# Kernel optimization log

Hardware: AMD Instinct MI355X
Metric: run time of the kernel (lower is better)

The kernel has to match this reference:

```python
import jax, jax.numpy as jnp
import numpy as np

T, N, H = 20, 1000000, 20  # timesteps, num_params (batch), lstm hidden dim


def setup_inputs() -> dict:
    key = jax.random.key(0)
    ks = jax.random.split(key, 7)
    s = 1.0 / np.sqrt(H)  # pytorch LSTM/Linear init scale (uniform bound); use gaussian of similar scale
    return {
        "grads": jax.random.normal(ks[0], (T, N), dtype=jnp.float32),
        "w_ih": jax.random.normal(ks[1], (4 * H, 1), dtype=jnp.float32) * s,
        "w_hh": jax.random.normal(ks[2], (4 * H, H), dtype=jnp.float32) * s,
        "b_ih": jax.random.normal(ks[3], (4 * H,), dtype=jnp.float32) * s,
        "b_hh": jax.random.normal(ks[4], (4 * H,), dtype=jnp.float32) * s,
        "w_fc": jax.random.normal(ks[5], (1, H), dtype=jnp.float32) * s,
        "b_fc": jax.random.normal(ks[6], (1,), dtype=jnp.float32) * s,
    }


def reference(grads, w_ih, w_hh, b_ih, b_hh, w_fc, b_fc):
    # grads: [T, N]; coordinate-wise LSTM: batch = N, input_size = 1, hidden = H.
    # PyTorch LSTM gate order: i, f, g, o.
    n = grads.shape[1]
    bias = b_ih + b_hh  # [4H]
    w_ih_v = w_ih[:, 0]  # [4H], input size is 1

    def step(carry, x_t):
        h, c = carry  # [N, H] each
        # gates: [N, 4H]
        gates = x_t[:, None] * w_ih_v[None, :] + h @ w_hh.T + bias
        i, f, g, o = jnp.split(gates, 4, axis=1)
        c_new = jax.nn.sigmoid(f) * c + jax.nn.sigmoid(i) * jnp.tanh(g)
        h_new = jax.nn.sigmoid(o) * jnp.tanh(c_new)
        out_t = h_new @ w_fc.T + b_fc  # [N, 1]
        return (h_new, c_new), out_t[:, 0]

    h0 = jnp.zeros((n, w_hh.shape[1]), dtype=grads.dtype)
    c0 = jnp.zeros((n, w_hh.shape[1]), dtype=grads.dtype)
    _, outs = jax.lax.scan(step, (h0, c0), grads)
    return outs  # [T, N], matches torch.cat(outputs) of [1, N] slices
```

## Files before the change

kernel.cpp:

```cpp
#include <hip/hip_runtime.h>

#define TT 20
#define HH 20

typedef float f32x4 __attribute__((ext_vector_type(4)));
typedef short bf16x8 __attribute__((ext_vector_type(8)));
typedef unsigned uint4v __attribute__((ext_vector_type(4)));

__device__ __forceinline__ short f2bf(float f) {
    unsigned u = __float_as_uint(f);
    unsigned r = (u + 0x7fffu + ((u >> 16) & 1u)) >> 16;
    return (short)r;
}

__device__ __forceinline__ unsigned pk_bf16(float a, float b) {
    unsigned r;
    asm("v_cvt_pk_bf16_f32 %0, %1, %2" : "=v"(r) : "v"(a), "v"(b));
    return r;
}

__device__ __forceinline__ void build_B(const float (&hn)[5][4], const float (&xv)[4],
                                        float xm, float om, bf16x8 (&Bhi)[4])
{
    #pragma unroll
    for (int b = 0; b < 4; ++b) {
        const float s7 = fmaf(xm, xv[b], om);
        uint4v uh;
        uh[0] = pk_bf16(hn[0][b], hn[1][b]);
        uh[1] = pk_bf16(hn[2][b], hn[3][b]);
        uh[2] = pk_bf16(hn[4][b], 0.0f);
        uh[3] = pk_bf16(0.0f, s7);
        Bhi[b] = __builtin_bit_cast(bf16x8, uh);
    }
}

__device__ __forceinline__ void nonlin(const f32x4 a, float& cst, float& hout,
                                       const float TLOG2E)
{
    const float ei = __builtin_amdgcn_exp2f(a[0]);
    const float ef = __builtin_amdgcn_exp2f(a[1]);
    const float eg = __builtin_amdgcn_exp2f(a[2]);
    const float eo = __builtin_amdgcn_exp2f(a[3]);
    const float pi = 1.0f + ei, pf = 1.0f + ef;
    const float pg = 1.0f + eg, po = 1.0f + eo;
    const float pig = pi * pg;
    const float r3  = __builtin_amdgcn_rcpf(pig * pf);
    const float cn  = fmaf(cst, pig, (eg - 1.0f) * pf) * r3;
    cst = cn;
    const float ec = __builtin_amdgcn_exp2f(TLOG2E * cn);
    const float pc = 1.0f + ec;
    hout = (ec - 1.0f) * __builtin_amdgcn_rcpf(po * pc);
}

__global__ __launch_bounds__(256, 3)
void coord_lstm_mfma(const float* __restrict__ grads,
                     const float* __restrict__ w_ih,
                     const float* __restrict__ w_hh,
                     const float* __restrict__ b_ih,
                     const float* __restrict__ b_hh,
                     const float* __restrict__ w_fc,
                     const float* __restrict__ b_fc,
                     float* __restrict__ out,
                     int N)
{
    const int lane = threadIdx.x & 63;
    const int g = lane >> 4;
    const int n = lane & 15;
    const long long base = ((long long)blockIdx.x * 4 + (threadIdx.x >> 6)) * 64;
    if (base >= N) return;

    const float LOG2E  = 1.4426950408889634f;
    const float TLOG2E = 2.8853900817779268f;
    const float xm = (g == 0) ? 1.0f : 0.0f;
    const float om = (g == 1) ? 1.0f : 0.0f;

    bf16x8 Ahi[6];
    #pragma unroll
    for (int tA = 0; tA < 6; ++tA) {
        bf16x8 ah;
        #pragma unroll
        for (int e = 0; e < 8; ++e) {
            float v = 0.0f;
            if (tA < 5) {
                const int r = 16 * tA + n;
                const int u_r = r >> 2;
                const int gate = r & 3;
                const float scale = (gate == 2) ? TLOG2E : -LOG2E;
                const int row_w = gate * HH + u_r;
                if (e < 5)       v = scale * w_hh[row_w * HH + (4 * e + g)];
                else if (e == 7) v = (g == 0) ? scale * w_ih[row_w]
                                   : (g == 1) ? scale * (b_ih[row_w] + b_hh[row_w]) : 0.0f;
            } else {
                if (e < 5)       v = (n == 0) ? w_fc[4 * e + g] : 0.0f;
                else if (e == 7) v = (g == 1 && n == 0) ? b_fc[0] : 0.0f;
            }
            ah[e] = f2bf(v);
        }
        Ahi[tA] = ah;
    }

    const f32x4 zero4 = {0.0f, 0.0f, 0.0f, 0.0f};

    long long cc[4]; bool wr[4];
    #pragma unroll
    for (int b = 0; b < 4; ++b) {
        long long c0 = base + 16 * b + n;
        wr[b] = (c0 < N);
        cc[b] = wr[b] ? c0 : (long long)(N - 1);
    }
    const float* gp0 = grads + cc[0];
    const float* gp1 = grads + cc[1];
    const float* gp2 = grads + cc[2];
    const float* gp3 = grads + cc[3];
    float* op0 = out + cc[0];
    float* op1 = out + cc[1];
    float* op2 = out + cc[2];
    float* op3 = out + cc[3];

    float c[5][4], hn[5][4];
    #pragma unroll
    for (int t5 = 0; t5 < 5; ++t5)
        #pragma unroll
        for (int b = 0; b < 4; ++b) { c[t5][b] = 0.0f; hn[t5][b] = 0.0f; }

    float xv[4];
    xv[0] = *gp0; gp0 += N;
    xv[1] = *gp1; gp1 += N;
    xv[2] = *gp2; gp2 += N;
    xv[3] = *gp3; gp3 += N;

    bf16x8 Bhi[4];
    build_B(hn, xv, xm, om, Bhi);

    #pragma unroll 1
    for (int t = 0; t < TT; ++t) {
        float xn[4];
        if (t < TT - 1) {
            xn[0] = *gp0; gp0 += N;
            xn[1] = *gp1; gp1 += N;
            xn[2] = *gp2; gp2 += N;
            xn[3] = *gp3; gp3 += N;
        } else {
            xn[0] = 0.0f; xn[1] = 0.0f; xn[2] = 0.0f; xn[3] = 0.0f;
        }

        #pragma unroll
        for (int tile = 0; tile < 5; ++tile) {
            f32x4 acc[4];
            #pragma unroll
            for (int b = 0; b < 4; ++b)
                acc[b] = __builtin_amdgcn_mfma_f32_16x16x32_bf16(Ahi[tile], Bhi[b], zero4, 0, 0, 0);
            #pragma unroll
            for (int b = 0; b < 4; ++b)
                nonlin(acc[b], c[tile][b], hn[tile][b], TLOG2E);
        }

        build_B(hn, xn, xm, om, Bhi);

        f32x4 ov[4];
        #pragma unroll
        for (int b = 0; b < 4; ++b)
            ov[b] = __builtin_amdgcn_mfma_f32_16x16x32_bf16(Ahi[5], Bhi[b], zero4, 0, 0, 0);

        if (g == 0) {
            if (wr[0]) *op0 = ov[0][0];
            if (wr[1]) *op1 = ov[1][0];
            if (wr[2]) *op2 = ov[2][0];
            if (wr[3]) *op3 = ov[3][0];
        }
        op0 += N; op1 += N; op2 += N; op3 += N;
    }
}

extern "C" void kernel_launch(void* const* d_in, const int* in_sizes, int n_in,
                              void* d_out, int out_size, void* d_ws, size_t ws_size,
                              hipStream_t stream) {
    const float* grads = (const float*)d_in[0];
    const float* w_ih  = (const float*)d_in[1];
    const float* w_hh  = (const float*)d_in[2];
    const float* b_ih  = (const float*)d_in[3];
    const float* b_hh  = (const float*)d_in[4];
    const float* w_fc  = (const float*)d_in[5];
    const float* b_fc  = (const float*)d_in[6];
    float* out = (float*)d_out;

    const int N = in_sizes[0] / TT;
    const long long waves = ((long long)N + 63) / 64;
    const int blocks = (int)((waves + 3) / 4);
    coord_lstm_mfma<<<blocks, 256, 0, stream>>>(grads, w_ih, w_hh, b_ih, b_hh,
                                                w_fc, b_fc, out, N);
}
```

Before: 372.4 us.

## Interleave LSTM per batch column, add aligned fast path, raise occupancy

```diff
diff --git a/kernel.cpp b/kernel.cpp
--- a/kernel.cpp
+++ b/kernel.cpp
@@ -4,6 +4,7 @@
 #define HH 20
 
 typedef float f32x4 __attribute__((ext_vector_type(4)));
+typedef float f32x2 __attribute__((ext_vector_type(2)));
 typedef short bf16x8 __attribute__((ext_vector_type(8)));
 typedef unsigned uint4v __attribute__((ext_vector_type(4)));
 
@@ -19,40 +20,38 @@
     return r;
 }
 
-__device__ __forceinline__ void build_B(const float (&hn)[5][4], const float (&xv)[4],
-                                        float xm, float om, bf16x8 (&Bhi)[4])
-{
-    #pragma unroll
-    for (int b = 0; b < 4; ++b) {
-        const float s7 = fmaf(xm, xv[b], om);
-        uint4v uh;
-        uh[0] = pk_bf16(hn[0][b], hn[1][b]);
-        uh[1] = pk_bf16(hn[2][b], hn[3][b]);
-        uh[2] = pk_bf16(hn[4][b], 0.0f);
-        uh[3] = pk_bf16(0.0f, s7);
-        Bhi[b] = __builtin_bit_cast(bf16x8, uh);
-    }
-}
-
-__device__ __forceinline__ void nonlin(const f32x4 a, float& cst, float& hout,
-                                       const float TLOG2E)
-{
-    const float ei = __builtin_amdgcn_exp2f(a[0]);
-    const float ef = __builtin_amdgcn_exp2f(a[1]);
-    const float eg = __builtin_amdgcn_exp2f(a[2]);
-    const float eo = __builtin_amdgcn_exp2f(a[3]);
-    const float pi = 1.0f + ei, pf = 1.0f + ef;
-    const float pg = 1.0f + eg, po = 1.0f + eo;
-    const float pig = pi * pg;
-    const float r3  = __builtin_amdgcn_rcpf(pig * pf);
-    const float cn  = fmaf(cst, pig, (eg - 1.0f) * pf) * r3;
-    cst = cn;
-    const float ec = __builtin_amdgcn_exp2f(TLOG2E * cn);
+__device__ __forceinline__ bf16x8 build_frag(const float (&h)[5], float s7) {
+    uint4v uh;
+    uh[0] = pk_bf16(h[0], h[1]);
+    uh[1] = pk_bf16(h[2], h[3]);
+    uh[2] = pk_bf16(h[4], 0.0f);
+    uh[3] = pk_bf16(0.0f, s7);
+    return __builtin_bit_cast(bf16x8, uh);
+}
+
+#define TLOG2E_C 2.8853900817779268f
+
+__device__ __forceinline__ void nonlin(const f32x4 a, float& cS, float& hout) {
+    f32x2 e_if, e_go;
+    e_if.x = __builtin_amdgcn_exp2f(a[0]);
+    e_if.y = __builtin_amdgcn_exp2f(a[1]);
+    e_go.x = __builtin_amdgcn_exp2f(a[2]);
+    e_go.y = __builtin_amdgcn_exp2f(a[3]);
+    const f32x2 one2 = {1.0f, 1.0f};
+    const f32x2 p_if = e_if + one2;
+    const f32x2 p_go = e_go + one2;
+    const float pig = p_if.x * p_go.x;
+    const float r3  = __builtin_amdgcn_rcpf(pig * p_if.y);
+    const float tn  = fmaf(e_go.x, TLOG2E_C, -TLOG2E_C) * p_if.y;
+    const float cnS = fmaf(cS, pig, tn) * r3;
+    cS = cnS;
+    const float ec = __builtin_amdgcn_exp2f(cnS);
     const float pc = 1.0f + ec;
-    hout = (ec - 1.0f) * __builtin_amdgcn_rcpf(po * pc);
-}
-
-__global__ __launch_bounds__(256, 3)
+    hout = (ec - 1.0f) * __builtin_amdgcn_rcpf(p_go.y * pc);
+}
+
+template <bool ALIGNED>
+__global__ __launch_bounds__(256, 4)
 void coord_lstm_mfma(const float* __restrict__ grads,
                      const float* __restrict__ w_ih,
                      const float* __restrict__ w_hh,
@@ -70,7 +69,7 @@
     if (base >= N) return;
 
     const float LOG2E  = 1.4426950408889634f;
-    const float TLOG2E = 2.8853900817779268f;
+    const float TLOG2E = TLOG2E_C;
     const float xm = (g == 0) ? 1.0f : 0.0f;
     const float om = (g == 1) ? 1.0f : 0.0f;
 
@@ -101,74 +100,105 @@
 
     const f32x4 zero4 = {0.0f, 0.0f, 0.0f, 0.0f};
 
+    const float* gp;
+    float* op;
     long long cc[4]; bool wr[4];
-    #pragma unroll
-    for (int b = 0; b < 4; ++b) {
-        long long c0 = base + 16 * b + n;
-        wr[b] = (c0 < N);
-        cc[b] = wr[b] ? c0 : (long long)(N - 1);
-    }
-    const float* gp0 = grads + cc[0];
-    const float* gp1 = grads + cc[1];
-    const float* gp2 = grads + cc[2];
-    const float* gp3 = grads + cc[3];
-    float* op0 = out + cc[0];
-    float* op1 = out + cc[1];
-    float* op2 = out + cc[2];
-    float* op3 = out + cc[3];
-
-    float c[5][4], hn[5][4];
+    const float *gpc0, *gpc1, *gpc2, *gpc3;
+    float *opc0, *opc1, *opc2, *opc3;
+    if constexpr (ALIGNED) {
+        gp = grads + base + n;
+        op = out + base + n;
+        (void)cc; (void)wr;
+        gpc0 = gpc1 = gpc2 = gpc3 = nullptr;
+        opc0 = opc1 = opc2 = opc3 = nullptr;
+    } else {
+        #pragma unroll
+        for (int b = 0; b < 4; ++b) {
+            long long c0 = base + 16 * b + n;
+            wr[b] = (c0 < N);
+            cc[b] = wr[b] ? c0 : (long long)(N - 1);
+        }
+        gpc0 = grads + cc[0]; gpc1 = grads + cc[1];
+        gpc2 = grads + cc[2]; gpc3 = grads + cc[3];
+        opc0 = out + cc[0]; opc1 = out + cc[1];
+        opc2 = out + cc[2]; opc3 = out + cc[3];
+        gp = nullptr; op = nullptr;
+    }
+
+    float cS[5][4];
     #pragma unroll
     for (int t5 = 0; t5 < 5; ++t5)
         #pragma unroll
-        for (int b = 0; b < 4; ++b) { c[t5][b] = 0.0f; hn[t5][b] = 0.0f; }
-
-    float xv[4];
-    xv[0] = *gp0; gp0 += N;
-    xv[1] = *gp1; gp1 += N;
-    xv[2] = *gp2; gp2 += N;
-    xv[3] = *gp3; gp3 += N;
-
-    bf16x8 Bhi[4];
-    build_B(hn, xv, xm, om, Bhi);
+        for (int b = 0; b < 4; ++b) cS[t5][b] = 0.0f;
+
+    bf16x8 B[4];
+    {
+        float x0[4];
+        if constexpr (ALIGNED) {
+            x0[0] = gp[0]; x0[1] = gp[16]; x0[2] = gp[32]; x0[3] = gp[48];
+            gp += N;
+        } else {
+            x0[0] = *gpc0; gpc0 += N;
+            x0[1] = *gpc1; gpc1 += N;
+            x0[2] = *gpc2; gpc2 += N;
+            x0[3] = *gpc3; gpc3 += N;
+        }
+        const float hz[5] = {0.0f, 0.0f, 0.0f, 0.0f, 0.0f};
+        #pragma unroll
+        for (int b = 0; b < 4; ++b)
+            B[b] = build_frag(hz, fmaf(xm, x0[b], om));
+    }
 
     #pragma unroll 1
     for (int t = 0; t < TT; ++t) {
         float xn[4];
-        if (t < TT - 1) {
-            xn[0] = *gp0; gp0 += N;
-            xn[1] = *gp1; gp1 += N;
-            xn[2] = *gp2; gp2 += N;
-            xn[3] = *gp3; gp3 += N;
+        if (t + 1 < TT) {
+            if constexpr (ALIGNED) {
+                xn[0] = gp[0]; xn[1] = gp[16]; xn[2] = gp[32]; xn[3] = gp[48];
+                gp += N;
+            } else {
+                xn[0] = *gpc0; gpc0 += N;
+                xn[1] = *gpc1; gpc1 += N;
+                xn[2] = *gpc2; gpc2 += N;
+                xn[3] = *gpc3; gpc3 += N;
+            }
         } else {
             xn[0] = 0.0f; xn[1] = 0.0f; xn[2] = 0.0f; xn[3] = 0.0f;
         }
 
         #pragma unroll
-        for (int tile = 0; tile < 5; ++tile) {
-            f32x4 acc[4];
-            #pragma unroll
-            for (int b = 0; b < 4; ++b)
-                acc[b] = __builtin_amdgcn_mfma_f32_16x16x32_bf16(Ahi[tile], Bhi[b], zero4, 0, 0, 0);
-            #pragma unroll
-            for (int b = 0; b < 4; ++b)
-                nonlin(acc[b], c[tile][b], hn[tile][b], TLOG2E);
-        }
-
-        build_B(hn, xn, xm, om, Bhi);
-
-        f32x4 ov[4];
-        #pragma unroll
-        for (int b = 0; b < 4; ++b)
-            ov[b] = __builtin_amdgcn_mfma_f32_16x16x32_bf16(Ahi[5], Bhi[b], zero4, 0, 0, 0);
-
-        if (g == 0) {
-            if (wr[0]) *op0 = ov[0][0];
-            if (wr[1]) *op1 = ov[1][0];
-            if (wr[2]) *op2 = ov[2][0];
-            if (wr[3]) *op3 = ov[3][0];
-        }
-        op0 += N; op1 += N; op2 += N; op3 += N;
+        for (int b = 0; b < 4; ++b) {
+            f32x4 a0 = __builtin_amdgcn_mfma_f32_16x16x32_bf16(Ahi[0], B[b], zero4, 0, 0, 0);
+            f32x4 a1 = __builtin_amdgcn_mfma_f32_16x16x32_bf16(Ahi[1], B[b], zero4, 0, 0, 0);
+            f32x4 a2 = __builtin_amdgcn_mfma_f32_16x16x32_bf16(Ahi[2], B[b], zero4, 0, 0, 0);
+            f32x4 a3 = __builtin_amdgcn_mfma_f32_16x16x32_bf16(Ahi[3], B[b], zero4, 0, 0, 0);
+            f32x4 a4 = __builtin_amdgcn_mfma_f32_16x16x32_bf16(Ahi[4], B[b], zero4, 0, 0, 0);
+
+            float hb[5];
+            nonlin(a0, cS[0][b], hb[0]);
+            nonlin(a1, cS[1][b], hb[1]);
+            nonlin(a2, cS[2][b], hb[2]);
+            nonlin(a3, cS[3][b], hb[3]);
+            nonlin(a4, cS[4][b], hb[4]);
+
+            B[b] = build_frag(hb, fmaf(xm, xn[b], om));
+
+            f32x4 ov = __builtin_amdgcn_mfma_f32_16x16x32_bf16(Ahi[5], B[b], zero4, 0, 0, 0);
+            if constexpr (ALIGNED) {
+                if (g == 0) op[16 * b] = ov[0];
+            } else {
+                if (g == 0 && wr[b]) {
+                    float* o = (b == 0) ? opc0 : (b == 1) ? opc1 : (b == 2) ? opc2 : opc3;
+                    *o = ov[0];
+                }
+            }
+        }
+
+        if constexpr (ALIGNED) {
+            op += N;
+        } else {
+            opc0 += N; opc1 += N; opc2 += N; opc3 += N;
+        }
     }
 }
 
@@ -187,6 +217,11 @@
     const int N = in_sizes[0] / TT;
     const long long waves = ((long long)N + 63) / 64;
     const int blocks = (int)((waves + 3) / 4);
-    coord_lstm_mfma<<<blocks, 256, 0, stream>>>(grads, w_ih, w_hh, b_ih, b_hh,
-                                                w_fc, b_fc, out, N);
-}
+    if (N % 64 == 0) {
+        coord_lstm_mfma<true><<<blocks, 256, 0, stream>>>(grads, w_ih, w_hh, b_ih, b_hh,
+                                                          w_fc, b_fc, out, N);
+    } else {
+        coord_lstm_mfma<false><<<blocks, 256, 0, stream>>>(grads, w_ih, w_hh, b_ih, b_hh,
+                                                           w_fc, b_fc, out, N);
+    }
+}
```

Result: faster. 361.6 us (-2.9%).
